# Optimization experiments

Hardware: AMD Instinct MI355X
Metric: run time of the kernel (lower is better)

## Reference

```python
import jax, jax.numpy as jnp
import numpy as np

ACTION_FEAT_DIM = 64
ACTION_EMB = 192
FUSION = 768
HID = 384
N_HEADS = 4
B, A = 2048, 64

gelu = lambda x: jax.nn.gelu(x, approximate=False)


def setup_inputs() -> dict:
    key = jax.random.key(0)
    ks = jax.random.split(key, 12)
    s = lambda fan_in: 1.0 / np.sqrt(fan_in)
    in_dim = ACTION_EMB + FUSION
    return {
        "action_feats": jax.random.normal(ks[0], (B, A, ACTION_FEAT_DIM), jnp.float32),
        "action_mask": jax.random.bernoulli(ks[1], 0.5, (B, A)),
        "fused": jax.random.normal(ks[2], (B, FUSION), jnp.float32),
        "phase_oh": jax.random.normal(ks[3], (B, 5), jnp.float32),
        # action encoder: Linear(64->192), GELU, Linear(192->192), GELU
        "We1": jax.random.uniform(ks[4], (ACTION_FEAT_DIM, ACTION_EMB), jnp.float32, -s(ACTION_FEAT_DIM), s(ACTION_FEAT_DIM)),
        "be1": jnp.zeros((ACTION_EMB,), jnp.float32),
        "We2": jax.random.uniform(ks[5], (ACTION_EMB, ACTION_EMB), jnp.float32, -s(ACTION_EMB), s(ACTION_EMB)),
        "be2": jnp.zeros((ACTION_EMB,), jnp.float32),
        # 4 phase heads: Linear(960->384), GELU, Linear(384->1), stacked on leading head axis
        "W1": jax.random.uniform(ks[6], (N_HEADS, in_dim, HID), jnp.float32, -s(in_dim), s(in_dim)),
        "b1": jnp.zeros((N_HEADS, HID), jnp.float32),
        "W2": jax.random.uniform(ks[7], (N_HEADS, HID), jnp.float32, -s(HID), s(HID)),
        "b2": jnp.zeros((N_HEADS,), jnp.float32),
    }


def reference(action_feats, action_mask, fused, phase_oh, We1, be1, We2, be2, W1, b1, W2, b2):
    bsz, act_count, _ = action_feats.shape
    # action encoder
    emb = gelu(gelu(action_feats @ We1 + be1) @ We2 + be2)          # [B,A,192]
    fused_rep = jnp.broadcast_to(fused[:, None, :], (bsz, act_count, fused.shape[-1]))
    inp = jnp.concatenate([emb, fused_rep], axis=-1)                 # [B,A,960]
    # dense compute of all 4 heads (faithful to original)
    h = gelu(jnp.einsum('bai,kio->bkao', inp, W1) + b1[None, :, None, :])  # [B,4,A,384]
    per_head = jnp.einsum('bkao,ko->bka', h, W2) + b2[None, :, None]       # [B,4,A]
    # phase routing: argmax over one-hot, phases >=3 map to head 3
    phase_idx = jnp.argmax(phase_oh, axis=-1)
    head_idx = jnp.where(phase_idx <= 2, phase_idx, 3)               # [B]
    logits = jnp.take_along_axis(per_head, head_idx[:, None, None], axis=1)[:, 0, :]  # [B,A]
    return jnp.where(action_mask, jnp.float32(-10000.0), logits)
```

## Files before the change

### kernel.cpp

```cpp
#include <hip/hip_runtime.h>


typedef __bf16 bf16x8 __attribute__((ext_vector_type(8)));
typedef unsigned short ushortx8 __attribute__((ext_vector_type(8)));
typedef float floatx4 __attribute__((ext_vector_type(4)));
typedef unsigned short u16;
typedef unsigned int u32;

#define B_SZ 2048
#define EMB 192
#define FUS 768
#define HID 384
#define INDIM 960
#define LDS_W 200

#define WS_FLAGS 0
#define WS_CNT 64
#define WS_HEAD 256
#define WS_LIST 8448
#define WS_WE1F 41216
#define WS_WE2F 65792
#define WS_W1F 139520
#define WS_FBF 3088640
#define WS_GSEL 6234368

__device__ __forceinline__ float bf2f(u16 u) {
  return __uint_as_float(((u32)u) << 16);
}
__device__ __forceinline__ u16 f2bf(float f) {
  u32 x = __float_as_uint(f);
  x += 0x7FFFu + ((x >> 16) & 1u);
  return (u16)(x >> 16);
}
__device__ __forceinline__ float ldf(const void* p, size_t i, int bf) {
  return bf ? bf2f(((const u16*)p)[i]) : ((const float*)p)[i];
}
__device__ __forceinline__ bf16x8 ld8(const void* p, size_t idx, int bf) {
  if (bf) return *reinterpret_cast<const bf16x8*>((const u16*)p + idx);
  const float* f = (const float*)p + idx;
  ushortx8 u;
#pragma unroll
  for (int i = 0; i < 8; ++i) u[i] = f2bf(f[i]);
  return __builtin_bit_cast(bf16x8, u);
}

__device__ __forceinline__ float gelu_f(float x) {
  float t = __expf(-1.702f * x);
  return x * __builtin_amdgcn_rcpf(1.0f + t);
}

__device__ __forceinline__ bool read_mask(const void* m, long long i, int fmt) {
  if (fmt == 0) return ((const int*)m)[i] != 0;
  if (fmt == 1) return ((const unsigned char*)m)[i] != 0;
  if (fmt == 2) return ((const u16*)m)[i] != 0;
  return ((const u32*)m)[i] != 0;
}

__device__ __forceinline__ int probe_bf(const void* act, int tid, int* s_bf) {
  if (tid < 64) {
    u32 w = ((const u32*)act)[tid];
    u32 h = w & 0xFFFFu;
    u32 e = (h >> 7) & 0xFFu;
    int pl = (h == 0u) || (e >= 90u && e <= 150u);
    unsigned long long nz = __ballot(h != 0u);
    unsigned long long pm = __ballot(pl);
    if (tid == 0) *s_bf = (nz != 0ULL && __popcll(pm) > 48) ? 1 : 0;
  }
  __syncthreads();
  return *s_bf;
}

#define NB_ROUTE 8
#define NB_FBF 512
#define NB_WF 744
__global__ void k_prep(const void* __restrict__ act, const void* __restrict__ phase,
                       const void* __restrict__ mask, const void* __restrict__ fused,
                       const void* __restrict__ we1, const void* __restrict__ we2,
                       const void* __restrict__ w1,
                       int* __restrict__ head_idx, int* __restrict__ flags,
                       int* __restrict__ cnt, int* __restrict__ list,
                       u16* __restrict__ we1f, u16* __restrict__ we2f,
                       u16* __restrict__ w1f, u16* __restrict__ fbf) {
  __shared__ int s_bf;
  const int tid = threadIdx.x;
  const int bx = blockIdx.x;
  const int bf = probe_bf(act, tid, &s_bf);

  if (bx < NB_ROUTE) {
    if (bx == 0 && tid == 0) flags[3] = bf;
    int t = bx * 256 + tid;
    float best = ldf(phase, (size_t)t * 5, bf);
    int bi = 0;
#pragma unroll
    for (int i = 1; i < 5; ++i) {
      float v = ldf(phase, (size_t)t * 5 + i, bf);
      if (v > best) { best = v; bi = i; }
    }
    int h = (bi <= 2) ? bi : 3;
    head_idx[t] = h;
    int pos = atomicAdd(&cnt[h], 1);
    list[h * 2048 + pos] = t;

    const u32* mw = (const u32*)mask;
    u32 vi = 0, vu = 0, en = 0;
#pragma unroll
    for (int j = 0; j < 16; ++j) {
      u32 w = mw[bx * 4096 + j * 256 + tid];
      vi |= (u32)(w > 1u);
      vu |= (u32)((w & 0xFEFEFEFEu) != 0u);
      en |= (u32)((w & 0x0000FFFFu) != 0u);
    }
    if (vi) atomicOr(&flags[0], 1);
    if (vu) atomicOr(&flags[1], 1);
    if (en) atomicOr(&flags[2], 1);
    return;
  }

  if (bx < NB_ROUTE + NB_FBF) {
    int gid = (bx - NB_ROUTE) * 256 + tid;
    if (bf) {
      const uint2* s = (const uint2*)fused;
      uint2* d = (uint2*)fbf;
      for (int i = gid; i < 393216; i += NB_FBF * 256) d[i] = s[i];
    } else {
      const float4* s = (const float4*)fused;
      uint2* d = (uint2*)fbf;
      for (int i = gid; i < 393216; i += NB_FBF * 256) {
        float4 v = s[i];
        uint2 o;
        o.x = (u32)f2bf(v.x) | ((u32)f2bf(v.y) << 16);
        o.y = (u32)f2bf(v.z) | ((u32)f2bf(v.w) << 16);
        d[i] = o;
      }
    }
    return;
  }

  int fid = (bx - NB_ROUTE - NB_FBF) * 256 + tid;
  int lane = fid & 63, rest = fid >> 6;
  int q = lane >> 4, nl = lane & 15;
  const void* src;
  u16* dst;
  int kk, col, ncols, dloc;
  size_t soff = 0;
  if (rest < 24) {
    src = we1; dst = we1f; dloc = fid;
    kk = rest & 1; col = (rest >> 1) * 16 + nl; ncols = EMB;
  } else if (rest < 96) {
    int r2 = rest - 24;
    src = we2; dst = we2f; dloc = (r2 << 6) | lane;
    kk = r2 % 6; col = (r2 / 6) * 16 + nl; ncols = EMB;
  } else {
    int r3 = rest - 96;
    src = w1; dst = w1f; dloc = (r3 << 6) | lane;
    kk = r3 % 30; int hn = r3 / 30;
    soff = (size_t)(hn / 24) * INDIM * HID;
    col = (hn % 24) * 16 + nl; ncols = HID;
  }
  int k0 = kk * 32 + q * 8;
  ushortx8 u;
#pragma unroll
  for (int j = 0; j < 8; ++j)
    u[j] = f2bf(ldf(src, soff + (size_t)(k0 + j) * ncols + col, bf));
  *reinterpret_cast<ushortx8*>(dst + (size_t)dloc * 8) = u;
}

__global__ __launch_bounds__(256, 4) void k_gall_sel(
    const u16* __restrict__ fbf, const u16* __restrict__ w1f,
    const void* __restrict__ b1, u16* __restrict__ gsel,
    const int* __restrict__ cnt, const int* __restrict__ list,
    const int* __restrict__ flags) {
  const int bf = flags[3];
  int c0 = cnt[0], c1 = cnt[1], c2 = cnt[2], c3 = cnt[3];
  int t0 = (c0 + 15) >> 4, t1 = (c1 + 15) >> 4, t2 = (c2 + 15) >> 4, t3 = (c3 + 15) >> 4;
  int x = blockIdx.x, h, tl;
  if (x < t0) { h = 0; tl = x; }
  else if (x < t0 + t1) { h = 1; tl = x - t0; }
  else if (x < t0 + t1 + t2) { h = 2; tl = x - t0 - t1; }
  else if (x < t0 + t1 + t2 + t3) { h = 3; tl = x - t0 - t1 - t2; }
  else return;
  int ch = (h == 0) ? c0 : (h == 1) ? c1 : (h == 2) ? c2 : c3;
  const int tid = threadIdx.x;
  const int w = tid >> 6, lane = tid & 63;
  const int nl = lane & 15, q = lane >> 4;

  int r = tl * 16 + nl;
  if (r >= ch) r = ch - 1;
  int bi = list[h * 2048 + r];
  const u16* arow = fbf + (size_t)bi * FUS;
  const int ntile = blockIdx.y * 4 + w;

  const floatx4 z4 = {0.f, 0.f, 0.f, 0.f};
  floatx4 acc = z4;
#pragma unroll 4
  for (int kk = 0; kk < 24; ++kk) {
    bf16x8 a = *reinterpret_cast<const bf16x8*>(arow + kk * 32 + q * 8);
    size_t fo = ((((size_t)h * 24 + ntile) * 30 + 6 + kk) * 64 + lane) * 8;
    bf16x8 bb = *reinterpret_cast<const bf16x8*>(w1f + fo);
    acc = __builtin_amdgcn_mfma_f32_16x16x32_bf16(a, bb, acc, 0, 0, 0);
  }
  int bi2[4];
#pragma unroll
  for (int rr = 0; rr < 4; ++rr) {
    int rm = tl * 16 + q * 4 + rr;
    if (rm >= ch) rm = ch - 1;
    bi2[rr] = list[h * 2048 + rm];
  }
  int col = ntile * 16 + nl;
  float bias = ldf(b1, (size_t)h * HID + col, bf);
#pragma unroll
  for (int rr = 0; rr < 4; ++rr)
    gsel[(size_t)bi2[rr] * HID + col] = f2bf(acc[rr] + bias);
}

__global__ __launch_bounds__(256, 4) void k_main(
    const void* __restrict__ act, const void* __restrict__ mask,
    const void* __restrict__ be1, const void* __restrict__ be2,
    const void* __restrict__ W2, const void* __restrict__ b2,
    const u16* __restrict__ we1f, const u16* __restrict__ we2f,
    const u16* __restrict__ w1f, const u16* __restrict__ gsel,
    const int* __restrict__ head_idx, const int* __restrict__ flags,
    void* __restrict__ out) {
  __shared__ __align__(16) u16 S[64 * LDS_W];
  __shared__ float red[256];
  const int b = blockIdx.x;
  const int tid = threadIdx.x;
  const int w = tid >> 6, lane = tid & 63;
  const int nl = lane & 15, q = lane >> 4;
  const int khead = head_idx[b];
  const int bf = flags[3];
  const floatx4 z4 = {0.f, 0.f, 0.f, 0.f};

  {
    floatx4 acc1[4][3];
#pragma unroll
    for (int mt = 0; mt < 4; ++mt)
#pragma unroll
      for (int nt = 0; nt < 3; ++nt) acc1[mt][nt] = z4;
#pragma unroll
    for (int kk = 0; kk < 2; ++kk) {
      bf16x8 a[4];
#pragma unroll
      for (int mt = 0; mt < 4; ++mt)
        a[mt] = ld8(act, ((size_t)b * 64 + mt * 16 + nl) * 64 + kk * 32 + q * 8, bf);
#pragma unroll
      for (int nt = 0; nt < 3; ++nt) {
        bf16x8 bfr = *reinterpret_cast<const bf16x8*>(
            we1f + (((w * 3 + nt) * 2 + kk) * 64 + lane) * 8);
#pragma unroll
        for (int mt = 0; mt < 4; ++mt)
          acc1[mt][nt] = __builtin_amdgcn_mfma_f32_16x16x32_bf16(a[mt], bfr, acc1[mt][nt], 0, 0, 0);
      }
    }
#pragma unroll
    for (int nt = 0; nt < 3; ++nt) {
      int col = w * 48 + nt * 16 + nl;
      float bias = ldf(be1, col, bf);
#pragma unroll
      for (int mt = 0; mt < 4; ++mt)
#pragma unroll
        for (int r = 0; r < 4; ++r)
          S[(mt * 16 + q * 4 + r) * LDS_W + col] = f2bf(gelu_f(acc1[mt][nt][r] + bias));
    }
  }
  __syncthreads();

  {
    floatx4 acc2[4][3];
#pragma unroll
    for (int mt = 0; mt < 4; ++mt)
#pragma unroll
      for (int nt = 0; nt < 3; ++nt) acc2[mt][nt] = z4;
#pragma unroll
    for (int kk = 0; kk < 6; ++kk) {
      bf16x8 a[4];
#pragma unroll
      for (int mt = 0; mt < 4; ++mt)
        a[mt] = *reinterpret_cast<const bf16x8*>(&S[(mt * 16 + nl) * LDS_W + kk * 32 + q * 8]);
#pragma unroll
      for (int nt = 0; nt < 3; ++nt) {
        bf16x8 bfr = *reinterpret_cast<const bf16x8*>(
            we2f + (((w * 3 + nt) * 6 + kk) * 64 + lane) * 8);
#pragma unroll
        for (int mt = 0; mt < 4; ++mt)
          acc2[mt][nt] = __builtin_amdgcn_mfma_f32_16x16x32_bf16(a[mt], bfr, acc2[mt][nt], 0, 0, 0);
      }
    }
    __syncthreads();
#pragma unroll
    for (int nt = 0; nt < 3; ++nt) {
      int col = w * 48 + nt * 16 + nl;
      float bias = ldf(be2, col, bf);
#pragma unroll
      for (int mt = 0; mt < 4; ++mt)
#pragma unroll
        for (int r = 0; r < 4; ++r)
          S[(mt * 16 + q * 4 + r) * LDS_W + col] = f2bf(gelu_f(acc2[mt][nt][r] + bias));
    }
  }
  __syncthreads();

  float partial[4][4];
#pragma unroll
  for (int mt = 0; mt < 4; ++mt)
#pragma unroll
    for (int r = 0; r < 4; ++r) partial[mt][r] = 0.f;
  const u16* grow = gsel + (size_t)b * HID;
#pragma unroll
  for (int half = 0; half < 2; ++half) {
    floatx4 acc3[4][3];
#pragma unroll
    for (int mt = 0; mt < 4; ++mt)
#pragma unroll
      for (int nt = 0; nt < 3; ++nt) acc3[mt][nt] = z4;
#pragma unroll
    for (int kk = 0; kk < 6; ++kk) {
      bf16x8 a[4];
#pragma unroll
      for (int mt = 0; mt < 4; ++mt)
        a[mt] = *reinterpret_cast<const bf16x8*>(&S[(mt * 16 + nl) * LDS_W + kk * 32 + q * 8]);
#pragma unroll
      for (int nt = 0; nt < 3; ++nt) {
        size_t fo = ((((size_t)khead * 24 + w * 6 + half * 3 + nt) * 30 + kk) * 64 + lane) * 8;
        bf16x8 bfr = *reinterpret_cast<const bf16x8*>(w1f + fo);
#pragma unroll
        for (int mt = 0; mt < 4; ++mt)
          acc3[mt][nt] = __builtin_amdgcn_mfma_f32_16x16x32_bf16(a[mt], bfr, acc3[mt][nt], 0, 0, 0);
      }
    }
#pragma unroll
    for (int nt = 0; nt < 3; ++nt) {
      int col = w * 96 + half * 48 + nt * 16 + nl;
      float g = bf2f(grow[col]);
      float w2c = ldf(W2, (size_t)khead * HID + col, bf);
#pragma unroll
      for (int mt = 0; mt < 4; ++mt)
#pragma unroll
        for (int r = 0; r < 4; ++r)
          partial[mt][r] += gelu_f(acc3[mt][nt][r] + g) * w2c;
    }
  }
#pragma unroll
  for (int off = 1; off < 16; off <<= 1)
#pragma unroll
    for (int mt = 0; mt < 4; ++mt)
#pragma unroll
      for (int r = 0; r < 4; ++r)
        partial[mt][r] += __shfl_xor(partial[mt][r], off, 16);
  if (nl == 0) {
#pragma unroll
    for (int mt = 0; mt < 4; ++mt)
#pragma unroll
      for (int r = 0; r < 4; ++r)
        red[w * 64 + mt * 16 + q * 4 + r] = partial[mt][r];
  }
  __syncthreads();

  if (tid < 64) {
    float s = red[tid] + red[64 + tid] + red[128 + tid] + red[192 + tid];
    int f0 = flags[0], f1 = flags[1], f2v = flags[2];
    int fmt = (f0 == 0) ? 0 : ((f1 == 0) ? 1 : ((f2v != 0) ? 2 : 3));
    float bb2 = ldf(b2, khead, bf);
    long long mi = (long long)b * 64 + tid;
    float v = read_mask(mask, mi, fmt) ? -10000.0f : (s + bb2);
    if (bf) ((u16*)out)[mi] = f2bf(v);
    else    ((float*)out)[mi] = v;
  }
}

extern "C" void kernel_launch(void* const* d_in, const int* in_sizes, int n_in,
                              void* d_out, int out_size, void* d_ws, size_t ws_size,
                              hipStream_t stream) {
  const void* act   = d_in[0];
  const void* mask  = d_in[1];
  const void* fused = d_in[2];
  const void* phase = d_in[3];
  const void* We1 = d_in[4];
  const void* be1 = d_in[5];
  const void* We2 = d_in[6];
  const void* be2 = d_in[7];
  const void* W1  = d_in[8];
  const void* b1  = d_in[9];
  const void* W2  = d_in[10];
  const void* b2  = d_in[11];
  char* ws = (char*)d_ws;
  int* flags    = (int*)(ws + WS_FLAGS);
  int* cnt      = (int*)(ws + WS_CNT);
  int* head_idx = (int*)(ws + WS_HEAD);
  int* list     = (int*)(ws + WS_LIST);
  u16* we1f = (u16*)(ws + WS_WE1F);
  u16* we2f = (u16*)(ws + WS_WE2F);
  u16* w1f  = (u16*)(ws + WS_W1F);
  u16* fbf  = (u16*)(ws + WS_FBF);
  u16* gsel = (u16*)(ws + WS_GSEL);

  hipMemsetAsync(flags, 0, 128, stream);
  k_prep<<<NB_ROUTE + NB_FBF + NB_WF, 256, 0, stream>>>(
      act, phase, mask, fused, We1, We2, W1,
      head_idx, flags, cnt, list, we1f, we2f, w1f, fbf);
  k_gall_sel<<<dim3(132, 6), 256, 0, stream>>>(fbf, w1f, b1, gsel, cnt, list, flags);
  k_main<<<B_SZ, 256, 0, stream>>>(act, mask, be1, be2, W2, b2, we1f, we2f,
                                   w1f, gsel, head_idx, flags, d_out);
}
```

Before: 203.8 us.

## Give each wave its own row tile in main kernel and drop memset via single-block routing

The main kernel now assigns each of the four waves a separate 16-row tile with all output columns, instead of splitting columns across waves. That removes the block barriers between stages and the shared-memory cross-wave reduction, but each wave now loads every weight fragment itself, so weight traffic per block is four times higher. Routing is rebuilt as a single block that computes per-head lists with a prefix scan rather than global atomics, and it writes flags directly, so the memset launch is gone. The fused-input conversion block count is halved.

Measured after the change: 243.7 us. 19.6% more time.

```diff
diff --git a/kernel.cpp b/kernel.cpp
--- a/kernel.cpp
+++ b/kernel.cpp
@@ -70,8 +70,7 @@
   return *s_bf;
 }
 
-#define NB_ROUTE 8
-#define NB_FBF 512
+#define NB_FBF 256
 #define NB_WF 744
 __global__ void k_prep(const void* __restrict__ act, const void* __restrict__ phase,
                        const void* __restrict__ mask, const void* __restrict__ fused,
@@ -86,38 +85,71 @@
   const int bx = blockIdx.x;
   const int bf = probe_bf(act, tid, &s_bf);
 
-  if (bx < NB_ROUTE) {
-    if (bx == 0 && tid == 0) flags[3] = bf;
-    int t = bx * 256 + tid;
-    float best = ldf(phase, (size_t)t * 5, bf);
-    int bi = 0;
-#pragma unroll
-    for (int i = 1; i < 5; ++i) {
-      float v = ldf(phase, (size_t)t * 5 + i, bf);
-      if (v > best) { best = v; bi = i; }
-    }
-    int h = (bi <= 2) ? bi : 3;
-    head_idx[t] = h;
-    int pos = atomicAdd(&cnt[h], 1);
-    list[h * 2048 + pos] = t;
-
+  if (bx == 0) {
+    __shared__ int sc[4][256];
+    __shared__ int sfl[3];
+    if (tid == 0) { sfl[0] = 0; sfl[1] = 0; sfl[2] = 0; }
+    int hh[8];
+    int myc[4] = {0, 0, 0, 0};
+#pragma unroll
+    for (int j = 0; j < 8; ++j) {
+      int b = tid * 8 + j;
+      float best = ldf(phase, (size_t)b * 5, bf);
+      int bi = 0;
+#pragma unroll
+      for (int i = 1; i < 5; ++i) {
+        float v = ldf(phase, (size_t)b * 5 + i, bf);
+        if (v > best) { best = v; bi = i; }
+      }
+      int h = (bi <= 2) ? bi : 3;
+      hh[j] = h;
+      head_idx[b] = h;
+      myc[h]++;
+    }
+#pragma unroll
+    for (int h = 0; h < 4; ++h) sc[h][tid] = myc[h];
+    __syncthreads();
+    for (int off = 1; off < 256; off <<= 1) {
+      int v[4];
+#pragma unroll
+      for (int h = 0; h < 4; ++h) v[h] = (tid >= off) ? sc[h][tid - off] : 0;
+      __syncthreads();
+#pragma unroll
+      for (int h = 0; h < 4; ++h) sc[h][tid] += v[h];
+      __syncthreads();
+    }
+    int start[4];
+#pragma unroll
+    for (int h = 0; h < 4; ++h) start[h] = sc[h][tid] - myc[h];
+#pragma unroll
+    for (int j = 0; j < 8; ++j) {
+      int h = hh[j];
+      list[h * 2048 + start[h]++] = tid * 8 + j;
+    }
+    if (tid == 0) {
+      flags[3] = bf;
+#pragma unroll
+      for (int h = 0; h < 4; ++h) cnt[h] = sc[h][255];
+    }
     const u32* mw = (const u32*)mask;
     u32 vi = 0, vu = 0, en = 0;
 #pragma unroll
-    for (int j = 0; j < 16; ++j) {
-      u32 w = mw[bx * 4096 + j * 256 + tid];
+    for (int j = 0; j < 128; ++j) {
+      u32 w = mw[j * 256 + tid];
       vi |= (u32)(w > 1u);
       vu |= (u32)((w & 0xFEFEFEFEu) != 0u);
       en |= (u32)((w & 0x0000FFFFu) != 0u);
     }
-    if (vi) atomicOr(&flags[0], 1);
-    if (vu) atomicOr(&flags[1], 1);
-    if (en) atomicOr(&flags[2], 1);
+    if (vi) atomicOr(&sfl[0], 1);
+    if (vu) atomicOr(&sfl[1], 1);
+    if (en) atomicOr(&sfl[2], 1);
+    __syncthreads();
+    if (tid == 0) { flags[0] = sfl[0]; flags[1] = sfl[1]; flags[2] = sfl[2]; }
     return;
   }
 
-  if (bx < NB_ROUTE + NB_FBF) {
-    int gid = (bx - NB_ROUTE) * 256 + tid;
+  if (bx < 1 + NB_FBF) {
+    int gid = (bx - 1) * 256 + tid;
     if (bf) {
       const uint2* s = (const uint2*)fused;
       uint2* d = (uint2*)fbf;
@@ -136,7 +168,7 @@
     return;
   }
 
-  int fid = (bx - NB_ROUTE - NB_FBF) * 256 + tid;
+  int fid = (bx - 1 - NB_FBF) * 256 + tid;
   int lane = fid & 63, rest = fid >> 6;
   int q = lane >> 4, nl = lane & 15;
   const void* src;
@@ -222,7 +254,6 @@
     const int* __restrict__ head_idx, const int* __restrict__ flags,
     void* __restrict__ out) {
   __shared__ __align__(16) u16 S[64 * LDS_W];
-  __shared__ float red[256];
   const int b = blockIdx.x;
   const int tid = threadIdx.x;
   const int w = tid >> 6, lane = tid & 63;
@@ -230,141 +261,102 @@
   const int khead = head_idx[b];
   const int bf = flags[3];
   const floatx4 z4 = {0.f, 0.f, 0.f, 0.f};
+  const int rb = w * 16;
 
   {
-    floatx4 acc1[4][3];
-#pragma unroll
-    for (int mt = 0; mt < 4; ++mt)
-#pragma unroll
-      for (int nt = 0; nt < 3; ++nt) acc1[mt][nt] = z4;
+    floatx4 acc1[12];
+#pragma unroll
+    for (int i = 0; i < 12; ++i) acc1[i] = z4;
 #pragma unroll
     for (int kk = 0; kk < 2; ++kk) {
-      bf16x8 a[4];
-#pragma unroll
-      for (int mt = 0; mt < 4; ++mt)
-        a[mt] = ld8(act, ((size_t)b * 64 + mt * 16 + nl) * 64 + kk * 32 + q * 8, bf);
-#pragma unroll
-      for (int nt = 0; nt < 3; ++nt) {
+      bf16x8 a = ld8(act, ((size_t)b * 64 + rb + nl) * 64 + kk * 32 + q * 8, bf);
+#pragma unroll
+      for (int nt = 0; nt < 12; ++nt) {
         bf16x8 bfr = *reinterpret_cast<const bf16x8*>(
-            we1f + (((w * 3 + nt) * 2 + kk) * 64 + lane) * 8);
-#pragma unroll
-        for (int mt = 0; mt < 4; ++mt)
-          acc1[mt][nt] = __builtin_amdgcn_mfma_f32_16x16x32_bf16(a[mt], bfr, acc1[mt][nt], 0, 0, 0);
-      }
-    }
-#pragma unroll
-    for (int nt = 0; nt < 3; ++nt) {
-      int col = w * 48 + nt * 16 + nl;
+            we1f + ((nt * 2 + kk) * 64 + lane) * 8);
+        acc1[nt] = __builtin_amdgcn_mfma_f32_16x16x32_bf16(a, bfr, acc1[nt], 0, 0, 0);
+      }
+    }
+#pragma unroll
+    for (int nt = 0; nt < 12; ++nt) {
+      int col = nt * 16 + nl;
       float bias = ldf(be1, col, bf);
 #pragma unroll
-      for (int mt = 0; mt < 4; ++mt)
-#pragma unroll
-        for (int r = 0; r < 4; ++r)
-          S[(mt * 16 + q * 4 + r) * LDS_W + col] = f2bf(gelu_f(acc1[mt][nt][r] + bias));
-    }
-  }
-  __syncthreads();
+      for (int r = 0; r < 4; ++r)
+        S[(rb + q * 4 + r) * LDS_W + col] = f2bf(gelu_f(acc1[nt][r] + bias));
+    }
+  }
 
   {
-    floatx4 acc2[4][3];
-#pragma unroll
-    for (int mt = 0; mt < 4; ++mt)
-#pragma unroll
-      for (int nt = 0; nt < 3; ++nt) acc2[mt][nt] = z4;
+    floatx4 acc2[12];
+#pragma unroll
+    for (int i = 0; i < 12; ++i) acc2[i] = z4;
 #pragma unroll
     for (int kk = 0; kk < 6; ++kk) {
-      bf16x8 a[4];
-#pragma unroll
-      for (int mt = 0; mt < 4; ++mt)
-        a[mt] = *reinterpret_cast<const bf16x8*>(&S[(mt * 16 + nl) * LDS_W + kk * 32 + q * 8]);
-#pragma unroll
-      for (int nt = 0; nt < 3; ++nt) {
+      bf16x8 a = *reinterpret_cast<const bf16x8*>(&S[(rb + nl) * LDS_W + kk * 32 + q * 8]);
+#pragma unroll
+      for (int nt = 0; nt < 12; ++nt) {
         bf16x8 bfr = *reinterpret_cast<const bf16x8*>(
-            we2f + (((w * 3 + nt) * 6 + kk) * 64 + lane) * 8);
-#pragma unroll
-        for (int mt = 0; mt < 4; ++mt)
-          acc2[mt][nt] = __builtin_amdgcn_mfma_f32_16x16x32_bf16(a[mt], bfr, acc2[mt][nt], 0, 0, 0);
-      }
-    }
-    __syncthreads();
-#pragma unroll
-    for (int nt = 0; nt < 3; ++nt) {
-      int col = w * 48 + nt * 16 + nl;
+            we2f + ((nt * 6 + kk) * 64 + lane) * 8);
+        acc2[nt] = __builtin_amdgcn_mfma_f32_16x16x32_bf16(a, bfr, acc2[nt], 0, 0, 0);
+      }
+    }
+#pragma unroll
+    for (int nt = 0; nt < 12; ++nt) {
+      int col = nt * 16 + nl;
       float bias = ldf(be2, col, bf);
 #pragma unroll
-      for (int mt = 0; mt < 4; ++mt)
-#pragma unroll
-        for (int r = 0; r < 4; ++r)
-          S[(mt * 16 + q * 4 + r) * LDS_W + col] = f2bf(gelu_f(acc2[mt][nt][r] + bias));
-    }
-  }
-  __syncthreads();
-
-  float partial[4][4];
-#pragma unroll
-  for (int mt = 0; mt < 4; ++mt)
-#pragma unroll
-    for (int r = 0; r < 4; ++r) partial[mt][r] = 0.f;
+      for (int r = 0; r < 4; ++r)
+        S[(rb + q * 4 + r) * LDS_W + col] = f2bf(gelu_f(acc2[nt][r] + bias));
+    }
+  }
+
+  float partial[4] = {0.f, 0.f, 0.f, 0.f};
   const u16* grow = gsel + (size_t)b * HID;
 #pragma unroll
   for (int half = 0; half < 2; ++half) {
-    floatx4 acc3[4][3];
-#pragma unroll
-    for (int mt = 0; mt < 4; ++mt)
-#pragma unroll
-      for (int nt = 0; nt < 3; ++nt) acc3[mt][nt] = z4;
+    floatx4 acc3[12];
+#pragma unroll
+    for (int i = 0; i < 12; ++i) acc3[i] = z4;
 #pragma unroll
     for (int kk = 0; kk < 6; ++kk) {
-      bf16x8 a[4];
-#pragma unroll
-      for (int mt = 0; mt < 4; ++mt)
-        a[mt] = *reinterpret_cast<const bf16x8*>(&S[(mt * 16 + nl) * LDS_W + kk * 32 + q * 8]);
-#pragma unroll
-      for (int nt = 0; nt < 3; ++nt) {
-        size_t fo = ((((size_t)khead * 24 + w * 6 + half * 3 + nt) * 30 + kk) * 64 + lane) * 8;
+      bf16x8 a = *reinterpret_cast<const bf16x8*>(&S[(rb + nl) * LDS_W + kk * 32 + q * 8]);
+#pragma unroll
+      for (int nt = 0; nt < 12; ++nt) {
+        int ntile = half * 12 + nt;
+        size_t fo = ((((size_t)khead * 24 + ntile) * 30 + kk) * 64 + lane) * 8;
         bf16x8 bfr = *reinterpret_cast<const bf16x8*>(w1f + fo);
-#pragma unroll
-        for (int mt = 0; mt < 4; ++mt)
-          acc3[mt][nt] = __builtin_amdgcn_mfma_f32_16x16x32_bf16(a[mt], bfr, acc3[mt][nt], 0, 0, 0);
-      }
-    }
-#pragma unroll
-    for (int nt = 0; nt < 3; ++nt) {
-      int col = w * 96 + half * 48 + nt * 16 + nl;
+        acc3[nt] = __builtin_amdgcn_mfma_f32_16x16x32_bf16(a, bfr, acc3[nt], 0, 0, 0);
+      }
+    }
+#pragma unroll
+    for (int nt = 0; nt < 12; ++nt) {
+      int col = (half * 12 + nt) * 16 + nl;
       float g = bf2f(grow[col]);
       float w2c = ldf(W2, (size_t)khead * HID + col, bf);
 #pragma unroll
-      for (int mt = 0; mt < 4; ++mt)
-#pragma unroll
-        for (int r = 0; r < 4; ++r)
-          partial[mt][r] += gelu_f(acc3[mt][nt][r] + g) * w2c;
+      for (int r = 0; r < 4; ++r)
+        partial[r] += gelu_f(acc3[nt][r] + g) * w2c;
     }
   }
 #pragma unroll
   for (int off = 1; off < 16; off <<= 1)
 #pragma unroll
-    for (int mt = 0; mt < 4; ++mt)
-#pragma unroll
-      for (int r = 0; r < 4; ++r)
-        partial[mt][r] += __shfl_xor(partial[mt][r], off, 16);
+    for (int r = 0; r < 4; ++r)
+      partial[r] += __shfl_xor(partial[r], off, 16);
+
   if (nl == 0) {
-#pragma unroll
-    for (int mt = 0; mt < 4; ++mt)
-#pragma unroll
-      for (int r = 0; r < 4; ++r)
-        red[w * 64 + mt * 16 + q * 4 + r] = partial[mt][r];
-  }
-  __syncthreads();
-
-  if (tid < 64) {
-    float s = red[tid] + red[64 + tid] + red[128 + tid] + red[192 + tid];
     int f0 = flags[0], f1 = flags[1], f2v = flags[2];
     int fmt = (f0 == 0) ? 0 : ((f1 == 0) ? 1 : ((f2v != 0) ? 2 : 3));
     float bb2 = ldf(b2, khead, bf);
-    long long mi = (long long)b * 64 + tid;
-    float v = read_mask(mask, mi, fmt) ? -10000.0f : (s + bb2);
-    if (bf) ((u16*)out)[mi] = f2bf(v);
-    else    ((float*)out)[mi] = v;
+#pragma unroll
+    for (int r = 0; r < 4; ++r) {
+      int row = rb + q * 4 + r;
+      long long mi = (long long)b * 64 + row;
+      float v = read_mask(mask, mi, fmt) ? -10000.0f : (partial[r] + bb2);
+      if (bf) ((u16*)out)[mi] = f2bf(v);
+      else    ((float*)out)[mi] = v;
+    }
   }
 }
 
@@ -394,8 +386,7 @@
   u16* fbf  = (u16*)(ws + WS_FBF);
   u16* gsel = (u16*)(ws + WS_GSEL);
 
-  hipMemsetAsync(flags, 0, 128, stream);
-  k_prep<<<NB_ROUTE + NB_FBF + NB_WF, 256, 0, stream>>>(
+  k_prep<<<1 + NB_FBF + NB_WF, 256, 0, stream>>>(
       act, phase, mask, fused, We1, We2, W1,
       head_idx, flags, cnt, list, we1f, we2f, w1f, fbf);
   k_gall_sel<<<dim3(132, 6), 256, 0, stream>>>(fbf, w1f, b1, gsel, cnt, list, flags);
```
